# Kernel tuning notes

Measured on AMD Instinct MI355X. Metric: run time of the kernel, lower is better.

The kernel has to match this reference:

```python
import jax, jax.numpy as jnp
import numpy as np

B, T, D = 4, 2048, 512
H, DK = 8, 64  # n_head, d_kv; inner_dim = H*DK = 512


def setup_inputs() -> dict:
    key = jax.random.key(0)
    ks = jax.random.split(key, 6)
    s = 1.0 / np.sqrt(D)
    return {
        "x": jax.random.normal(ks[0], (B, T, D), dtype=jnp.float32),
        "mask": jnp.zeros((B, 1, 1, T), dtype=jnp.float32),
        "position_bias": jax.random.normal(ks[1], (1, H, T, T), dtype=jnp.float32),
        "Wq": jax.random.normal(ks[2], (D, D), dtype=jnp.float32) * s,
        "Wk": jax.random.normal(ks[3], (D, D), dtype=jnp.float32) * s,
        "Wv": jax.random.normal(ks[4], (D, D), dtype=jnp.float32) * s,
        "Wo": jax.random.normal(ks[5], (D, D), dtype=jnp.float32) * s,
    }


def reference(x, mask, position_bias, Wq, Wk, Wv, Wo):
    # Linear projections (torch nn.Linear: y = x @ W.T), split into heads.
    q = (x @ Wq.T).reshape(B, T, H, DK).transpose(0, 2, 1, 3)  # [B,H,T,DK]
    k = (x @ Wk.T).reshape(B, T, H, DK).transpose(0, 2, 1, 3)  # [B,H,S,DK]
    v = (x @ Wv.T).reshape(B, T, H, DK).transpose(0, 2, 1, 3)  # [B,H,S,DK]
    # T5: no 1/sqrt(d_k) scaling; additive position bias + mask before softmax.
    scores = jnp.einsum("bhtd,bhsd->bhts", q, k) + position_bias + mask
    attn = jax.nn.softmax(scores.astype(jnp.float32), axis=-1).astype(q.dtype)
    # dropout is identity at inference
    y = jnp.einsum("bhts,bhsd->bhtd", attn, v)  # [B,H,T,DK]
    y = y.transpose(0, 2, 1, 3).reshape(B, T, H * DK)
    return y @ Wo.T
```

## Files before the change

kernel.cpp:

```cpp
#include <hip/hip_runtime.h>
#include <stdint.h>

typedef unsigned short u16;
typedef __attribute__((ext_vector_type(8))) _Float16 half8;
typedef __attribute__((ext_vector_type(4))) float f32x4;

#define L2E 1.4426950408889634f

#define NTOK 8192
#define DIM  512
#define TT   2048

__device__ __forceinline__ u16 f2h(float f) {
  _Float16 h = (_Float16)f;
  return __builtin_bit_cast(u16, h);
}

__device__ __forceinline__ void async16(const void* g, void* l) {
  __builtin_amdgcn_global_load_lds(
      (const __attribute__((address_space(1))) unsigned int*)g,
      (__attribute__((address_space(3))) unsigned int*)l, 16, 0, 0);
}

__global__ __launch_bounds__(256) void k_convert(
    const float* __restrict__ x, const float* __restrict__ wq,
    const float* __restrict__ wk, const float* __restrict__ wv,
    const float* __restrict__ wo, u16* __restrict__ xb) {
  size_t i = ((size_t)blockIdx.x * 256 + threadIdx.x) * 8;
  const float* src;
  u16* dst;
  size_t off;
  if (i < 4194304) {
    src = x; dst = xb; off = i;
  } else {
    size_t j = i - 4194304;
    int w = (int)(j >> 18);
    off = j & 262143;
    src = (w == 0) ? wq : (w == 1) ? wk : (w == 2) ? wv : wo;
    dst = xb + 4194304 + (size_t)w * 262144;
  }
  float4 a = *(const float4*)(src + off);
  float4 b = *(const float4*)(src + off + 4);
  uint4 pk;
  pk.x = (unsigned)f2h(a.x) | ((unsigned)f2h(a.y) << 16);
  pk.y = (unsigned)f2h(a.z) | ((unsigned)f2h(a.w) << 16);
  pk.z = (unsigned)f2h(b.x) | ((unsigned)f2h(b.y) << 16);
  pk.w = (unsigned)f2h(b.z) | ((unsigned)f2h(b.w) << 16);
  *(uint4*)(dst + off) = pk;
}

template <bool VSWAP>
__global__ __launch_bounds__(256) void k_proj(
    const u16* __restrict__ A, const u16* __restrict__ Wb,
    u16* __restrict__ Db) {
  const int tid = threadIdx.x;
  const int wave = tid >> 6, lane = tid & 63;
  const int quad = lane >> 4, l16 = lane & 15;
  const int wr = wave >> 1, wc = wave & 1;
  const int m0 = blockIdx.x * 128, n0 = blockIdx.y * 128;

  const u16* W;
  u16* D;
  if (VSWAP) {
    W = Wb + 2 * 262144;
    D = Db + 2 * (size_t)4194304;
  } else {
    int z = blockIdx.z;
    W = Wb + (size_t)z * 262144;
    D = Db + (size_t)z * 4194304;
  }

  __shared__ __align__(16) u16 As[128 * 64];
  __shared__ __align__(16) u16 Bs[128 * 64];

  f32x4 acc[4][4];
  for (int rt = 0; rt < 4; ++rt)
    for (int ct = 0; ct < 4; ++ct) acc[rt][ct] = (f32x4){0.f, 0.f, 0.f, 0.f};

  for (int kb = 0; kb < 8; ++kb) {
    const int k0 = kb * 64;
    for (int r = 0; r < 4; ++r) {
      int cid = r * 256 + tid;
      int row = cid >> 3, cl = cid & 7, cg = cl ^ (row & 7);
      async16(A + (size_t)(m0 + row) * DIM + k0 + cg * 8,
              &As[(r * 256 + wave * 64) * 8]);
    }
    for (int r = 0; r < 4; ++r) {
      int cid = r * 256 + tid;
      int row = cid >> 3, cl = cid & 7, cg = cl ^ (row & 7);
      async16(W + (size_t)(n0 + row) * DIM + k0 + cg * 8,
              &Bs[(r * 256 + wave * 64) * 8]);
    }
    __syncthreads();
    for (int kc = 0; kc < 2; ++kc) {
      half8 af[4], wf[4];
      for (int rt = 0; rt < 4; ++rt) {
        int row = wr * 64 + rt * 16 + l16;
        int c = (kc * 4 + quad) ^ (row & 7);
        af[rt] = *(const half8*)&As[row * 64 + c * 8];
      }
      for (int ct = 0; ct < 4; ++ct) {
        int row = wc * 64 + ct * 16 + l16;
        int c = (kc * 4 + quad) ^ (row & 7);
        wf[ct] = *(const half8*)&Bs[row * 64 + c * 8];
      }
      for (int rt = 0; rt < 4; ++rt)
        for (int ct = 0; ct < 4; ++ct)
          acc[rt][ct] = VSWAP
              ? __builtin_amdgcn_mfma_f32_16x16x32_f16(wf[ct], af[rt],
                                                       acc[rt][ct], 0, 0, 0)
              : __builtin_amdgcn_mfma_f32_16x16x32_f16(af[rt], wf[ct],
                                                       acc[rt][ct], 0, 0, 0);
    }
    __syncthreads();
  }

  for (int rt = 0; rt < 4; ++rt)
    for (int ct = 0; ct < 4; ++ct)
      for (int reg = 0; reg < 4; ++reg) {
        float v = acc[rt][ct][reg];
        if (!VSWAP) {
          int gm = m0 + wr * 64 + rt * 16 + quad * 4 + reg;
          int gn = n0 + wc * 64 + ct * 16 + l16;
          int bb = gm >> 11, t = gm & 2047, hh = gn >> 6, dk = gn & 63;
          D[(((size_t)(bb * 8 + hh) * TT + t) << 6) + dk] = f2h(v);
        } else {
          int feat = n0 + wc * 64 + ct * 16 + quad * 4 + reg;
          int tok  = m0 + wr * 64 + rt * 16 + l16;
          int bb = tok >> 11, t = tok & 2047, hh = feat >> 6, dk = feat & 63;
          D[(((size_t)(bb * 8 + hh) << 6) + dk) * TT + t] = f2h(v);
        }
      }
}

__global__ __launch_bounds__(256) void k_ogemm(
    const u16* __restrict__ A, const u16* __restrict__ W,
    float* __restrict__ Df) {
  const int tid = threadIdx.x;
  const int wave = tid >> 6, lane = tid & 63;
  const int quad = lane >> 4, l16 = lane & 15;
  const int wr = wave >> 1, wc = wave & 1;
  const int m0 = blockIdx.x * 64, n0 = blockIdx.y * 128;

  __shared__ __align__(16) u16 As[64 * 64];
  __shared__ __align__(16) u16 Bs[128 * 64];

  f32x4 acc[2][4];
  for (int rt = 0; rt < 2; ++rt)
    for (int ct = 0; ct < 4; ++ct) acc[rt][ct] = (f32x4){0.f, 0.f, 0.f, 0.f};

  for (int kb = 0; kb < 8; ++kb) {
    const int k0 = kb * 64;
    for (int r = 0; r < 2; ++r) {
      int cid = r * 256 + tid;
      int row = cid >> 3, cl = cid & 7, cg = cl ^ (row & 7);
      async16(A + (size_t)(m0 + row) * DIM + k0 + cg * 8,
              &As[(r * 256 + wave * 64) * 8]);
    }
    for (int r = 0; r < 4; ++r) {
      int cid = r * 256 + tid;
      int row = cid >> 3, cl = cid & 7, cg = cl ^ (row & 7);
      async16(W + (size_t)(n0 + row) * DIM + k0 + cg * 8,
              &Bs[(r * 256 + wave * 64) * 8]);
    }
    __syncthreads();
    for (int kc = 0; kc < 2; ++kc) {
      half8 af[2], wf[4];
      for (int rt = 0; rt < 2; ++rt) {
        int row = wr * 32 + rt * 16 + l16;
        int c = (kc * 4 + quad) ^ (row & 7);
        af[rt] = *(const half8*)&As[row * 64 + c * 8];
      }
      for (int ct = 0; ct < 4; ++ct) {
        int row = wc * 64 + ct * 16 + l16;
        int c = (kc * 4 + quad) ^ (row & 7);
        wf[ct] = *(const half8*)&Bs[row * 64 + c * 8];
      }
      for (int rt = 0; rt < 2; ++rt)
        for (int ct = 0; ct < 4; ++ct)
          acc[rt][ct] = __builtin_amdgcn_mfma_f32_16x16x32_f16(
              af[rt], wf[ct], acc[rt][ct], 0, 0, 0);
    }
    __syncthreads();
  }

  for (int rt = 0; rt < 2; ++rt)
    for (int ct = 0; ct < 4; ++ct)
      for (int reg = 0; reg < 4; ++reg) {
        int gm = m0 + wr * 32 + rt * 16 + quad * 4 + reg;
        int gn = n0 + wc * 64 + ct * 16 + l16;
        Df[(size_t)gm * DIM + gn] = acc[rt][ct][reg];
      }
}

__global__ __launch_bounds__(256, 4) void k_attn(
    const u16* __restrict__ Q, const u16* __restrict__ K,
    const u16* __restrict__ Vt, const float* __restrict__ bias,
    const float* __restrict__ mask, u16* __restrict__ Y) {
  const int tid = threadIdx.x;
  const int wv = tid >> 6;
  const int lane = tid & 63;
  const int quad = lane >> 4;
  const int l16 = lane & 15;

  const int bx = blockIdx.x;
  const int h = bx & 7;
  const int lid = bx >> 3;
  const int b = lid >> 5;
  const int qt = lid & 31;
  const int bh = b * 8 + h;
  const int q0 = qt * 64;

  __shared__ __align__(16) u16 Ks[2][64 * 64];
  __shared__ __align__(16) u16 Vs[2][64 * 64];
  __shared__ __align__(16) u16 Pl[64 * 64];

  const int qrow = q0 + wv * 16 + l16;
  half8 qf[2];
  {
    size_t qoff = ((size_t)bh * TT + qrow) * 64;
    qf[0] = *(const half8*)(Q + qoff + quad * 8);
    qf[1] = *(const half8*)(Q + qoff + 32 + quad * 8);
  }

  const float* brow = bias + (size_t)h * TT * TT + (size_t)qrow * TT + quad * 4;
  const float* mrow = mask + (size_t)b * TT + quad * 4;

  float m_i = -1e30f, l_i = 0.f;
  f32x4 oacc[4];
  for (int ct = 0; ct < 4; ++ct) oacc[ct] = (f32x4){0.f, 0.f, 0.f, 0.f};

  const int prow = wv * 16 + l16;
  const int r7x = (l16 & 7) << 4;
  char* plb = (char*)Pl + prow * 128;

#define STAGE(BUF, S0)                                                  \
  for (int r = 0; r < 2; ++r) {                                         \
    int cid = r * 256 + tid;                                            \
    int row = cid >> 3, cl = cid & 7, cg = cl ^ (row & 7);              \
    async16(K + ((size_t)bh * TT + (S0) + row) * 64 + cg * 8,           \
            &Ks[BUF][(r * 256 + wv * 64) * 8]);                         \
    async16(Vt + ((size_t)(bh * 64 + row)) * TT + (S0) + cg * 8,        \
            &Vs[BUF][(r * 256 + wv * 64) * 8]);                         \
  }

  f32x4 bA[4], bB[4];
  STAGE(0, 0);
  for (int ct = 0; ct < 4; ++ct) bA[ct] = *(const f32x4*)(brow + ct * 16);
  __syncthreads();

#define TILE(ST, CUR, BU, BF)                                               \
  {                                                                         \
    const int s0 = (ST) * 64;                                               \
    if ((ST) < 31) {                                                        \
      STAGE((CUR) ^ 1, s0 + 64);                                            \
      for (int ct = 0; ct < 4; ++ct)                                        \
        BF[ct] = *(const f32x4*)(brow + s0 + 64 + ct * 16);                 \
    }                                                                       \
    f32x4 mL[4];                                                            \
    for (int ct = 0; ct < 4; ++ct)                                          \
      mL[ct] = *(const f32x4*)(mrow + s0 + ct * 16);                        \
                                \
    f32x4 sacc[4];                                                          \
    for (int ct = 0; ct < 4; ++ct) sacc[ct] = (f32x4){0.f, 0.f, 0.f, 0.f};  \
    __builtin_amdgcn_s_setprio(1);                                          \
    for (int kc = 0; kc < 2; ++kc) {                                        \
      half8 kf[4];                                                          \
      for (int ct = 0; ct < 4; ++ct) {                                      \
        int row = ct * 16 + l16;                                            \
        int c = (kc * 4 + quad) ^ (row & 7);                                \
        kf[ct] = *(const half8*)&Ks[CUR][row * 64 + c * 8];                 \
      }                                                                     \
      for (int ct = 0; ct < 4; ++ct)                                        \
        sacc[ct] = __builtin_amdgcn_mfma_f32_16x16x32_f16(kf[ct], qf[kc],   \
                                                          sacc[ct], 0, 0, 0); \
    }                                                                       \
    __builtin_amdgcn_s_setprio(0);                                          \
    float sv[4][4];                                                         \
    for (int ct = 0; ct < 4; ++ct)                                          \
      for (int rg = 0; rg < 4; ++rg)                                        \
        sv[ct][rg] = sacc[ct][rg] + BU[ct][rg] + mL[ct][rg];                \
                     \
    float mc0 = fmaxf(fmaxf(sv[0][0], sv[0][1]), fmaxf(sv[0][2], sv[0][3])); \
    float mc1 = fmaxf(fmaxf(sv[1][0], sv[1][1]), fmaxf(sv[1][2], sv[1][3])); \
    float mc2 = fmaxf(fmaxf(sv[2][0], sv[2][1]), fmaxf(sv[2][2], sv[2][3])); \
    float mc3 = fmaxf(fmaxf(sv[3][0], sv[3][1]), fmaxf(sv[3][2], sv[3][3])); \
    float mx = fmaxf(fmaxf(mc0, mc1), fmaxf(mc2, mc3));                     \
    mx = fmaxf(mx, __shfl_xor(mx, 16));                                     \
    mx = fmaxf(mx, __shfl_xor(mx, 32));                                     \
    if (!__all(mx <= m_i + 8.f)) {                                          \
      float mnew = fmaxf(m_i, mx);                                          \
      float alpha = __builtin_amdgcn_exp2f((m_i - mnew) * L2E);             \
      l_i *= alpha;                                                         \
      m_i = mnew;                                                           \
      for (int ct = 0; ct < 4; ++ct) {                                      \
        oacc[ct][0] *= alpha; oacc[ct][1] *= alpha;                         \
        oacc[ct][2] *= alpha; oacc[ct][3] *= alpha;                         \
      }                                                                     \
    }                                                                       \
    float nl2e = m_i * L2E;                                                 \
    float rs = 0.f;                                                         \
    for (int ct = 0; ct < 4; ++ct)                                          \
      for (int rg = 0; rg < 4; ++rg) {                                      \
        float p = __builtin_amdgcn_exp2f(sv[ct][rg] * L2E - nl2e);          \
        sv[ct][rg] = p;                                                     \
        rs += p;                                                            \
      }                                                                     \
    rs += __shfl_xor(rs, 16);                                               \
    rs += __shfl_xor(rs, 32);                                               \
    l_i += rs;                                                              \
                            \
    for (int ct = 0; ct < 4; ++ct) {                                        \
      uint2 pk;                                                             \
      pk.x = (unsigned)f2h(sv[ct][0]) | ((unsigned)f2h(sv[ct][1]) << 16);   \
      pk.y = (unsigned)f2h(sv[ct][2]) | ((unsigned)f2h(sv[ct][3]) << 16);   \
      *(uint2*)(plb + ((ct * 32 + quad * 8) ^ r7x)) = pk;                   \
    }                                                                       \
    asm volatile("s_waitcnt lgkmcnt(0)" ::: "memory");                      \
    __builtin_amdgcn_sched_barrier(0);                                      \
                            \
    __builtin_amdgcn_s_setprio(1);                                          \
    for (int kc = 0; kc < 2; ++kc) {                                        \
      half8 pf = *(const half8*)(plb + ((kc * 64 + quad * 16) ^ r7x));      \
      half8 vf[4];                                                          \
      for (int ct = 0; ct < 4; ++ct) {                                      \
        int row = ct * 16 + l16;                                            \
        int c = (kc * 4 + quad) ^ (row & 7);                                \
        vf[ct] = *(const half8*)&Vs[CUR][row * 64 + c * 8];                 \
      }                                                                     \
      for (int ct = 0; ct < 4; ++ct)                                        \
        oacc[ct] = __builtin_amdgcn_mfma_f32_16x16x32_f16(vf[ct], pf,       \
                                                          oacc[ct], 0, 0, 0); \
    }                                                                       \
    __builtin_amdgcn_s_setprio(0);                                          \
    __syncthreads();                                                        \
  }

  for (int st2 = 0; st2 < 16; ++st2) {
    TILE(2 * st2, 0, bA, bB);
    TILE(2 * st2 + 1, 1, bB, bA);
  }
#undef TILE
#undef STAGE

  float inv = 1.f / l_i;
  size_t ybase = ((size_t)(b * TT + qrow)) * DIM + h * 64 + quad * 4;
  for (int ct = 0; ct < 4; ++ct) {
    uint2 pk;
    pk.x = (unsigned)f2h(oacc[ct][0] * inv) |
           ((unsigned)f2h(oacc[ct][1] * inv) << 16);
    pk.y = (unsigned)f2h(oacc[ct][2] * inv) |
           ((unsigned)f2h(oacc[ct][3] * inv) << 16);
    *(uint2*)(Y + ybase + ct * 16) = pk;
  }
}

extern "C" void kernel_launch(void* const* d_in, const int* in_sizes, int n_in,
                              void* d_out, int out_size, void* d_ws, size_t ws_size,
                              hipStream_t stream) {
  const float* x    = (const float*)d_in[0];
  const float* mask = (const float*)d_in[1];
  const float* bias = (const float*)d_in[2];
  const float* Wq   = (const float*)d_in[3];
  const float* Wk   = (const float*)d_in[4];
  const float* Wv   = (const float*)d_in[5];
  const float* Wo   = (const float*)d_in[6];
  (void)Wk; (void)Wv;

  u16* xb  = (u16*)d_ws;
  u16* wb  = xb + 4194304;
  u16* qkv = wb + 4 * 262144;
  u16* yb  = qkv + 3 * (size_t)4194304;

  k_convert<<<2560, 256, 0, stream>>>(x, Wq, Wk, Wv, Wo, xb);
  k_proj<false><<<dim3(64, 4, 2), 256, 0, stream>>>(xb, wb, qkv);
  k_proj<true><<<dim3(64, 4), 256, 0, stream>>>(xb, wb, qkv);
  k_attn<<<1024, 256, 0, stream>>>(qkv, qkv + 4194304,
                                   qkv + 2 * (size_t)4194304, bias, mask, yb);
  k_ogemm<<<dim3(128, 4), 256, 0, stream>>>(yb, wb + 3 * 262144, (float*)d_out);
}
```

Measured before the change: 342.4 us.

## Redistribute softmax P via ds_bpermute instead of LDS; always rescale; vectorize QKV stores

The attention kernel no longer writes the P tile to shared memory and reads it back in MFMA operand layout. It packs P to half pairs in registers and moves them between lanes with ds_bpermute, dropping the Pl buffer and its waitcnt/sched barrier. The lazy conditional rescale of the running max is replaced by an unconditional rescale every tile, which adds multiplies but removes a wave vote and a branch. The non-transposed QKV projection path now swaps MFMA operands so each lane can store four contiguous fp16 values as one 8-byte store.

```diff
diff --git a/kernel.cpp b/kernel.cpp
--- a/kernel.cpp
+++ b/kernel.cpp
@@ -106,31 +106,34 @@
       }
       for (int rt = 0; rt < 4; ++rt)
         for (int ct = 0; ct < 4; ++ct)
-          acc[rt][ct] = VSWAP
-              ? __builtin_amdgcn_mfma_f32_16x16x32_f16(wf[ct], af[rt],
-                                                       acc[rt][ct], 0, 0, 0)
-              : __builtin_amdgcn_mfma_f32_16x16x32_f16(af[rt], wf[ct],
-                                                       acc[rt][ct], 0, 0, 0);
+          acc[rt][ct] = __builtin_amdgcn_mfma_f32_16x16x32_f16(
+              wf[ct], af[rt], acc[rt][ct], 0, 0, 0);
     }
     __syncthreads();
   }
 
   for (int rt = 0; rt < 4; ++rt)
-    for (int ct = 0; ct < 4; ++ct)
-      for (int reg = 0; reg < 4; ++reg) {
-        float v = acc[rt][ct][reg];
-        if (!VSWAP) {
-          int gm = m0 + wr * 64 + rt * 16 + quad * 4 + reg;
-          int gn = n0 + wc * 64 + ct * 16 + l16;
-          int bb = gm >> 11, t = gm & 2047, hh = gn >> 6, dk = gn & 63;
-          D[(((size_t)(bb * 8 + hh) * TT + t) << 6) + dk] = f2h(v);
-        } else {
+    for (int ct = 0; ct < 4; ++ct) {
+      if (!VSWAP) {
+        int feat0 = n0 + wc * 64 + ct * 16 + quad * 4;
+        int tok   = m0 + wr * 64 + rt * 16 + l16;
+        int bb = tok >> 11, t = tok & 2047, hh = feat0 >> 6, dk0 = feat0 & 63;
+        uint2 pk;
+        pk.x = (unsigned)f2h(acc[rt][ct][0]) |
+               ((unsigned)f2h(acc[rt][ct][1]) << 16);
+        pk.y = (unsigned)f2h(acc[rt][ct][2]) |
+               ((unsigned)f2h(acc[rt][ct][3]) << 16);
+        *(uint2*)&D[(((size_t)(bb * 8 + hh) * TT + t) << 6) + dk0] = pk;
+      } else {
+        for (int reg = 0; reg < 4; ++reg) {
           int feat = n0 + wc * 64 + ct * 16 + quad * 4 + reg;
           int tok  = m0 + wr * 64 + rt * 16 + l16;
           int bb = tok >> 11, t = tok & 2047, hh = feat >> 6, dk = feat & 63;
-          D[(((size_t)(bb * 8 + hh) << 6) + dk) * TT + t] = f2h(v);
+          D[(((size_t)(bb * 8 + hh) << 6) + dk) * TT + t] =
+              f2h(acc[rt][ct][reg]);
         }
       }
+    }
 }
 
 __global__ __launch_bounds__(256) void k_ogemm(
@@ -213,7 +216,6 @@
 
   __shared__ __align__(16) u16 Ks[2][64 * 64];
   __shared__ __align__(16) u16 Vs[2][64 * 64];
-  __shared__ __align__(16) u16 Pl[64 * 64];
 
   const int qrow = q0 + wv * 16 + l16;
   half8 qf[2];
@@ -230,9 +232,9 @@
   f32x4 oacc[4];
   for (int ct = 0; ct < 4; ++ct) oacc[ct] = (f32x4){0.f, 0.f, 0.f, 0.f};
 
-  const int prow = wv * 16 + l16;
-  const int r7x = (l16 & 7) << 4;
-  char* plb = (char*)Pl + prow * 128;
+  const int iA = ((((lane >> 4) & 1) << 5) + l16) << 2;
+  const int iB = iA + 64;
+  const bool hi = lane >= 32;
 
 #define STAGE(BUF, S0)                                                  \
   for (int r = 0; r < 2; ++r) {                                         \
@@ -260,7 +262,7 @@
     f32x4 mL[4];                                                            \
     for (int ct = 0; ct < 4; ++ct)                                          \
       mL[ct] = *(const f32x4*)(mrow + s0 + ct * 16);                        \
-                                \
+             \
     f32x4 sacc[4];                                                          \
     for (int ct = 0; ct < 4; ++ct) sacc[ct] = (f32x4){0.f, 0.f, 0.f, 0.f};  \
     __builtin_amdgcn_s_setprio(1);                                          \
@@ -280,7 +282,7 @@
     for (int ct = 0; ct < 4; ++ct)                                          \
       for (int rg = 0; rg < 4; ++rg)                                        \
         sv[ct][rg] = sacc[ct][rg] + BU[ct][rg] + mL[ct][rg];                \
-                     \
+                 \
     float mc0 = fmaxf(fmaxf(sv[0][0], sv[0][1]), fmaxf(sv[0][2], sv[0][3])); \
     float mc1 = fmaxf(fmaxf(sv[1][0], sv[1][1]), fmaxf(sv[1][2], sv[1][3])); \
     float mc2 = fmaxf(fmaxf(sv[2][0], sv[2][1]), fmaxf(sv[2][2], sv[2][3])); \
@@ -288,17 +290,9 @@
     float mx = fmaxf(fmaxf(mc0, mc1), fmaxf(mc2, mc3));                     \
     mx = fmaxf(mx, __shfl_xor(mx, 16));                                     \
     mx = fmaxf(mx, __shfl_xor(mx, 32));                                     \
-    if (!__all(mx <= m_i + 8.f)) {                                          \
-      float mnew = fmaxf(m_i, mx);                                          \
-      float alpha = __builtin_amdgcn_exp2f((m_i - mnew) * L2E);             \
-      l_i *= alpha;                                                         \
-      m_i = mnew;                                                           \
-      for (int ct = 0; ct < 4; ++ct) {                                      \
-        oacc[ct][0] *= alpha; oacc[ct][1] *= alpha;                         \
-        oacc[ct][2] *= alpha; oacc[ct][3] *= alpha;                         \
-      }                                                                     \
-    }                                                                       \
-    float nl2e = m_i * L2E;                                                 \
+    float mnew = fmaxf(m_i, mx);                                            \
+    float alpha = __builtin_amdgcn_exp2f((m_i - mnew) * L2E);               \
+    float nl2e = mnew * L2E;                                                \
     float rs = 0.f;                                                         \
     for (int ct = 0; ct < 4; ++ct)                                          \
       for (int rg = 0; rg < 4; ++rg) {                                      \
@@ -308,20 +302,35 @@
       }                                                                     \
     rs += __shfl_xor(rs, 16);                                               \
     rs += __shfl_xor(rs, 32);                                               \
-    l_i += rs;                                                              \
-                            \
+    l_i = l_i * alpha + rs;                                                 \
+    m_i = mnew;                                                             \
     for (int ct = 0; ct < 4; ++ct) {                                        \
-      uint2 pk;                                                             \
-      pk.x = (unsigned)f2h(sv[ct][0]) | ((unsigned)f2h(sv[ct][1]) << 16);   \
-      pk.y = (unsigned)f2h(sv[ct][2]) | ((unsigned)f2h(sv[ct][3]) << 16);   \
-      *(uint2*)(plb + ((ct * 32 + quad * 8) ^ r7x)) = pk;                   \
-    }                                                                       \
-    asm volatile("s_waitcnt lgkmcnt(0)" ::: "memory");                      \
-    __builtin_amdgcn_sched_barrier(0);                                      \
-                            \
+      oacc[ct][0] *= alpha; oacc[ct][1] *= alpha;                           \
+      oacc[ct][2] *= alpha; oacc[ct][3] *= alpha;                           \
+    }                                                                       \
+     \
+    unsigned u[4][2];                                                       \
+    for (int ct = 0; ct < 4; ++ct) {                                        \
+      u[ct][0] = (unsigned)f2h(sv[ct][0]) | ((unsigned)f2h(sv[ct][1]) << 16); \
+      u[ct][1] = (unsigned)f2h(sv[ct][2]) | ((unsigned)f2h(sv[ct][3]) << 16); \
+    }                                                                       \
+      \
     __builtin_amdgcn_s_setprio(1);                                          \
     for (int kc = 0; kc < 2; ++kc) {                                        \
-      half8 pf = *(const half8*)(plb + ((kc * 64 + quad * 16) ^ r7x));      \
+      int pA0 = __builtin_amdgcn_ds_bpermute(iA, (int)u[kc * 2][0]);        \
+      int pA1 = __builtin_amdgcn_ds_bpermute(iA, (int)u[kc * 2][1]);        \
+      int pB0 = __builtin_amdgcn_ds_bpermute(iB, (int)u[kc * 2][0]);        \
+      int pB1 = __builtin_amdgcn_ds_bpermute(iB, (int)u[kc * 2][1]);        \
+      int qA0 = __builtin_amdgcn_ds_bpermute(iA, (int)u[kc * 2 + 1][0]);    \
+      int qA1 = __builtin_amdgcn_ds_bpermute(iA, (int)u[kc * 2 + 1][1]);    \
+      int qB0 = __builtin_amdgcn_ds_bpermute(iB, (int)u[kc * 2 + 1][0]);    \
+      int qB1 = __builtin_amdgcn_ds_bpermute(iB, (int)u[kc * 2 + 1][1]);    \
+      uint4 R;                                                              \
+      R.x = (unsigned)(hi ? qA0 : pA0);                                     \
+      R.y = (unsigned)(hi ? qA1 : pA1);                                     \
+      R.z = (unsigned)(hi ? qB0 : pB0);                                     \
+      R.w = (unsigned)(hi ? qB1 : pB1);                                     \
+      half8 pf = __builtin_bit_cast(half8, R);                              \
       half8 vf[4];                                                          \
       for (int ct = 0; ct < 4; ++ct) {                                      \
         int row = ct * 16 + l16;                                            \
@@ -333,7 +342,7 @@
                                                           oacc[ct], 0, 0, 0); \
     }                                                                       \
     __builtin_amdgcn_s_setprio(0);                                          \
-    __syncthreads();                                                        \
+    __syncthreads();     \
   }
 
   for (int st2 = 0; st2 < 16; ++st2) {
```

Measured after the change: 348.4 us. About the same (+1.8%).
